# Performance work log

Hardware: AMD Instinct MI355X
Metric: run time of the kernel (lower is better)

Reference implementation:

```python
import jax, jax.numpy as jnp
import numpy as np
from jax import lax

B, C, H, W, P = 16, 256, 64, 64, 4
EPS = 1e-5


def setup_inputs() -> dict:
    key = jax.random.key(0)
    ks = jax.random.split(key, 16)
    s = 0.05
    d = {
        'rgb': jax.random.normal(ks[0], (B, C, H, W), jnp.float32),
        'th': jax.random.normal(ks[1], (B, C, H, W), jnp.float32),
        'q_w': jax.random.normal(ks[2], (C, C), jnp.float32) * s,
        'q_b': jax.random.normal(ks[3], (C,), jnp.float32) * s,
        'kvr_w': jax.random.normal(ks[4], (2 * C, C), jnp.float32) * s,
        'kvr_b': jax.random.normal(ks[5], (2 * C,), jnp.float32) * s,
        'kvt_w': jax.random.normal(ks[6], (2 * C, C), jnp.float32) * s,
        'kvt_b': jax.random.normal(ks[7], (2 * C,), jnp.float32) * s,
        'offr_w': jax.random.normal(ks[8], (2 * P, C, 3, 3), jnp.float32) * s,
        'offr_b': jax.random.normal(ks[9], (2 * P,), jnp.float32) * s,
        'offt_w': jax.random.normal(ks[10], (2 * P, C, 3, 3), jnp.float32) * s,
        'offt_b': jax.random.normal(ks[11], (2 * P,), jnp.float32) * s,
        'out_w': jax.random.normal(ks[12], (C, 2 * C), jnp.float32) * s,
        'out_b': jax.random.normal(ks[13], (C,), jnp.float32) * s,
        'gamma': jnp.ones((C,), jnp.float32),
        'beta': jnp.zeros((C,), jnp.float32),
    }
    return d


def conv1x1(x, w, b):
    # x: [B,Ci,H,W], w: [Co,Ci] -> [B,Co,H,W]
    return jnp.einsum('bchw,oc->bohw', x, w) + b[None, :, None, None]


def conv3x3(x, w, b):
    y = lax.conv_general_dilated(x, w, (1, 1), 'SAME',
                                 dimension_numbers=('NCHW', 'OIHW', 'NCHW'))
    return y + b[None, :, None, None]


def deform_sample(feat, offset):
    # feat: [B,C,H,W]; offset: [B,2P,H,W] (pixel-unit offsets, (x,y) pairs)
    Bs, Cs, Hs, Ws = feat.shape
    off = offset.reshape(Bs, -1, 2, Hs, Ws)  # [B,P,2,H,W]
    # base grid in [-1,1], align_corners=True convention
    gy = jnp.linspace(-1.0, 1.0, Hs)[None, None, :, None]
    gx = jnp.linspace(-1.0, 1.0, Ws)[None, None, None, :]
    grid_x = gx + off[:, :, 0] / (Ws / 2.0)  # [B,P,H,W]
    grid_y = gy + off[:, :, 1] / (Hs / 2.0)
    # normalized -> pixel coords (align_corners=True)
    x = (grid_x + 1.0) * (Ws - 1) / 2.0
    y = (grid_y + 1.0) * (Hs - 1) / 2.0
    x0 = jnp.floor(x)
    y0 = jnp.floor(y)
    wx = x - x0
    wy = y - y0
    feat_flat = feat.reshape(Bs, Cs, Hs * Ws)

    def corner(xi, yi, wgt):
        valid = (xi >= 0) & (xi < Ws) & (yi >= 0) & (yi < Hs)  # zeros padding
        xc = jnp.clip(xi, 0, Ws - 1).astype(jnp.int32)
        yc = jnp.clip(yi, 0, Hs - 1).astype(jnp.int32)
        idx = (yc * Ws + xc).reshape(Bs, 1, -1)  # [B,1,P*H*W]
        g = jnp.take_along_axis(feat_flat, jnp.broadcast_to(idx, (Bs, Cs, idx.shape[-1])), axis=2)
        g = g.reshape(Bs, Cs, -1, Hs, Ws)  # [B,C,P,H,W]
        w_eff = (wgt * valid.astype(feat.dtype))[:, None]  # [B,1,P,H,W]
        return g * w_eff

    x0i = x0.astype(jnp.int32)
    y0i = y0.astype(jnp.int32)
    out = (corner(x0i, y0i, (1 - wx) * (1 - wy))
           + corner(x0i + 1, y0i, wx * (1 - wy))
           + corner(x0i, y0i + 1, (1 - wx) * wy)
           + corner(x0i + 1, y0i + 1, wx * wy))
    return out.mean(axis=2)  # mean over P -> [B,C,H,W]


def batchnorm_train(x, gamma, beta):
    mu = x.mean(axis=(0, 2, 3), keepdims=True)
    var = x.var(axis=(0, 2, 3), keepdims=True)
    xn = (x - mu) * lax.rsqrt(var + EPS)
    return xn * gamma[None, :, None, None] + beta[None, :, None, None]


def reference(rgb, th, q_w, q_b, kvr_w, kvr_b, kvt_w, kvt_b,
              offr_w, offr_b, offt_w, offt_b, out_w, out_b, gamma, beta):
    q_rgb = conv1x1(rgb, q_w, q_b)
    q_th = conv1x1(th, q_w, q_b)
    kv_rgb = conv1x1(rgb, kvr_w, kvr_b)
    kv_th = conv1x1(th, kvt_w, kvt_b)
    v_rgb = kv_rgb[:, C:]  # k_rgb = kv_rgb[:, :C] is unused downstream
    v_th = kv_th[:, C:]
    off_rgb2th = conv3x3(th, offr_w, offr_b)
    off_th2rgb = conv3x3(rgb, offt_w, offt_b)
    v_rgb2th = deform_sample(v_rgb, off_rgb2th)
    v_th2rgb = deform_sample(v_th, off_th2rgb)
    attn_rgb = jax.nn.sigmoid(q_rgb) * v_th2rgb
    attn_th = jax.nn.sigmoid(q_th) * v_rgb2th
    fused = conv1x1(jnp.concatenate([attn_rgb, attn_th], axis=1), out_w, out_b)
    return batchnorm_train(fused + 0.5 * (rgb + th), gamma, beta)
```

## Files before the change

### kernel.cpp

```cpp
#include <hip/hip_runtime.h>

typedef __bf16 bf16x8 __attribute__((ext_vector_type(8)));
typedef float  f32x4  __attribute__((ext_vector_type(4)));

constexpr int Bn = 16, Cn = 256, Hn = 64, Wn = 64, HWn = 64 * 64;
constexpr int Ntot = Bn * HWn;

#define DEV static __device__ __forceinline__

DEV unsigned short f2bf(float f) {
  unsigned u = __builtin_bit_cast(unsigned, f);
  u += 0x7fffu + ((u >> 16) & 1u);
  return (unsigned short)(u >> 16);
}
DEV float bf2f(unsigned short s) {
  unsigned u = ((unsigned)s) << 16;
  return __builtin_bit_cast(float, u);
}
DEV bf16x8 asbf(uint4 u) { return __builtin_bit_cast(bf16x8, u); }

__global__ void k_prep(const float* qw, const float* kvrw, const float* kvtw,
                       const float* offrw, const float* offtw, const float* outw,
                       unsigned short* Aqv, unsigned short* Aoff, unsigned short* Aout) {
  int idx = blockIdx.x * 256 + threadIdx.x;
  if (idx < 2 * 512 * 256) {
    int t = idx >> 17; int r = idx & 131071; int o = r >> 8; int c = r & 255;
    float v = (o < 256) ? qw[o * 256 + c] : (t ? kvtw[o * 256 + c] : kvrw[o * 256 + c]);
    Aqv[idx] = f2bf(v);
    return;
  }
  idx -= 2 * 512 * 256;
  if (idx < 2 * 16 * 2304) {
    int t = idx / 36864; int r = idx % 36864;
    int o = r / 2304; int rc = r % 2304; int tap = rc >> 8; int c = rc & 255;
    const float* w = t ? offtw : offrw;
    float v = (o < 8) ? w[(o * 256 + c) * 9 + tap] : 0.f;
    Aoff[idx] = f2bf(v);
    return;
  }
  idx -= 2 * 16 * 2304;
  if (idx < 256 * 512) Aout[idx] = f2bf(outw[idx]);
}

__global__ void k_transpose(const float* rgb, const float* th, unsigned short* xT) {
  int bi = blockIdx.x;
  int ct = bi & 3;
  int nt = (bi >> 2) & 63;
  int b  = (bi >> 8) & 15;
  int t  = bi >> 12;
  const float* src = t ? th : rgb;
  int c0 = ct * 64, n0 = nt * 64;
  __shared__ float tile[64][65];
  int tid = threadIdx.x;
  int nl = tid & 63, cg = tid >> 6;
#pragma unroll
  for (int i = 0; i < 16; i++) {
    int c = cg * 16 + i;
    tile[c][nl] = src[(size_t)(b * 256 + c0 + c) * HWn + n0 + nl];
  }
  __syncthreads();
  int pr = tid >> 2, sg = tid & 3;
  unsigned short tmp[16];
#pragma unroll
  for (int j = 0; j < 16; j++) tmp[j] = f2bf(tile[sg * 16 + j][pr]);
  unsigned short* dst = xT + (size_t)t * Ntot * 256 +
                        (size_t)(b * HWn + n0 + pr) * 256 + c0 + sg * 16;
  *(uint4*)(dst)     = *(const uint4*)(tmp);
  *(uint4*)(dst + 8) = *(const uint4*)(tmp + 8);
}

__global__ __launch_bounds__(512, 2) void k_qv(
    const unsigned short* Aqv, const unsigned short* xT,
    const float* qb, const float* kvrb, const float* kvtb,
    unsigned short* qs, unsigned short* vv) {
  __shared__ unsigned short smem[32768];
  int t  = blockIdx.z;
  int mt = blockIdx.y;
  int nt = blockIdx.x;
  int swznt = ((nt & 7) << 6) | (nt >> 3);
  int o0 = mt * 128;
  int n0 = swznt * 128;
  int tid = threadIdx.x;
  const unsigned short* Aq = Aqv + t * 512 * 256;
  const unsigned short* Xg = xT + (size_t)t * Ntot * 256 + (size_t)n0 * 256;

  auto stage = [&](int kb, int bb) {
    unsigned short* As = smem + bb * 8192;
    unsigned short* Xs = smem + 16384 + bb * 8192;
#pragma unroll
    for (int i = 0; i < 2; i++) {
      int cid = tid + i * 512;
      int row = cid >> 3, seg = cid & 7;
      int ss = seg ^ (row & 7);
      *(uint4*)(&As[row * 64 + seg * 8]) =
          *(const uint4*)(Aq + (size_t)(o0 + row) * 256 + kb * 64 + ss * 8);
    }
#pragma unroll
    for (int i = 0; i < 2; i++) {
      int cid = tid + i * 512;
      int row = cid >> 3, seg = cid & 7;
      int ss = seg ^ (row & 7);
      *(uint4*)(&Xs[row * 64 + seg * 8]) =
          *(const uint4*)(Xg + (size_t)row * 256 + kb * 64 + ss * 8);
    }
  };

  int w = __builtin_amdgcn_readfirstlane(tid >> 6);
  int lane = tid & 63;
  int wo = w & 1, wn = w >> 1;
  int r16 = lane & 15, q4 = lane >> 4;

  f32x4 acc[4][2];
#pragma unroll
  for (int a = 0; a < 4; a++) { acc[a][0] = f32x4{0.f,0.f,0.f,0.f}; acc[a][1] = f32x4{0.f,0.f,0.f,0.f}; }

  stage(0, 0);
  __syncthreads();
#pragma unroll
  for (int kb = 0; kb < 4; kb++) {
    if (kb < 3) stage(kb + 1, (kb + 1) & 1);
    const unsigned short* As = smem + (kb & 1) * 8192;
    const unsigned short* Xs = smem + 16384 + (kb & 1) * 8192;
#pragma unroll
    for (int ks = 0; ks < 2; ks++) {
      uint4 af[4], bfr[2];
#pragma unroll
      for (int oi = 0; oi < 4; oi++) {
        int row = wo * 64 + oi * 16 + r16;
        int seg = (ks * 4 + q4) ^ (row & 7);
        af[oi] = *(const uint4*)(&As[row * 64 + seg * 8]);
      }
#pragma unroll
      for (int ni = 0; ni < 2; ni++) {
        int row = wn * 32 + ni * 16 + r16;
        int seg = (ks * 4 + q4) ^ (row & 7);
        bfr[ni] = *(const uint4*)(&Xs[row * 64 + seg * 8]);
      }
#pragma unroll
      for (int oi = 0; oi < 4; oi++)
#pragma unroll
        for (int ni = 0; ni < 2; ni++)
          acc[oi][ni] = __builtin_amdgcn_mfma_f32_16x16x32_bf16(
              asbf(af[oi]), asbf(bfr[ni]), acc[oi][ni], 0, 0, 0);
    }
    __syncthreads();
  }

  bool isq = (mt < 2);
  const float* bias = isq ? qb : (t ? kvtb : kvrb);
  float4 bv[4];
#pragma unroll
  for (int oi = 0; oi < 4; oi++)
    bv[oi] = *(const float4*)(&bias[o0 + wo * 64 + oi * 16 + q4 * 4]);
#pragma unroll
  for (int oi = 0; oi < 4; oi++) {
    int ol = wo * 64 + oi * 16 + q4 * 4;
#pragma unroll
    for (int ni = 0; ni < 2; ni++) {
      int nl = wn * 32 + ni * 16 + r16;
      unsigned short pk[4];
#pragma unroll
      for (int j = 0; j < 4; j++) {
        float val = acc[oi][ni][j] + ((const float*)&bv[oi])[j];
        if (isq) val = 1.f / (1.f + __expf(-val));
        pk[j] = f2bf(val);
      }
      *(uint2*)(&smem[nl * 132 + ol]) = *(const uint2*)(pk);
    }
  }
  __syncthreads();
  unsigned short* outp = (isq ? qs : vv) + (size_t)t * Ntot * 256 + (mt & 1) * 128;
#pragma unroll
  for (int pass = 0; pass < 4; pass++) {
    int nl = pass * 32 + (tid >> 4);
    int c  = tid & 15;
    uint4 vq = *(const uint4*)(&smem[nl * 132 + c * 8]);
    *(uint4*)(outp + (size_t)(n0 + nl) * 256 + c * 8) = vq;
  }
}

__global__ void k_off(const unsigned short* Aoff, const unsigned short* xT,
                      const float* offrb, const float* offtb, float* offo) {
  int t  = blockIdx.y;
  int bh = blockIdx.x;
  int b = bh >> 6, h = bh & 63;
  int tid = threadIdx.x, lane = tid & 63, w = tid >> 6;
  int r16 = lane & 15, q4 = lane >> 4;
  int wl = w * 16 + r16;
  const unsigned short* Aw  = Aoff + t * 36864;
  const unsigned short* xin = xT + (size_t)(t ? 0 : 1) * Ntot * 256;
  f32x4 acc = {0.f, 0.f, 0.f, 0.f};
#pragma unroll
  for (int tap = 0; tap < 9; tap++) {
    int dy = tap / 3 - 1, dx = tap % 3 - 1;
    int hh = h + dy, ww = wl + dx;
    bool valid = (hh >= 0 && hh < 64 && ww >= 0 && ww < 64);
    const unsigned short* bsrc =
        xin + (size_t)((b * 64 + (valid ? hh : 0)) * 64 + (valid ? ww : 0)) * 256 + q4 * 8;
#pragma unroll
    for (int ks = 0; ks < 8; ks++) {
      uint4 a = *(const uint4*)(Aw + (r16 * 9 + tap) * 256 + ks * 32 + q4 * 8);
      uint4 bv;
      if (valid) bv = *(const uint4*)(bsrc + ks * 32);
      else { bv.x = 0; bv.y = 0; bv.z = 0; bv.w = 0; }
      acc = __builtin_amdgcn_mfma_f32_16x16x32_bf16(asbf(a), asbf(bv), acc, 0, 0, 0);
    }
  }
  if (lane < 32) {
    const float* ob = t ? offtb : offrb;
    int n = (b * 64 + h) * 64 + wl;
    float4 r;
    r.x = acc[0] + ob[q4 * 4 + 0];
    r.y = acc[1] + ob[q4 * 4 + 1];
    r.z = acc[2] + ob[q4 * 4 + 2];
    r.w = acc[3] + ob[q4 * 4 + 3];
    *(float4*)(offo + (size_t)t * Ntot * 8 + (size_t)n * 8 + q4 * 4) = r;
  }
}

__global__ void k_gather(const unsigned short* qs, const unsigned short* vv,
                         const float* offo, unsigned short* concat) {
  int tid = threadIdx.x;
  int bi  = blockIdx.x;
  int pass = blockIdx.y;
  int swz = ((bi & 7) << 9) | (bi >> 3);
  int chunk = tid & 15, pixL = tid >> 4;
  int n = swz * 16 + pixL;
  int b = n >> 12;
  int h = (n >> 6) & 63, pix = n & 63;
  const unsigned short* vsrc = vv + (size_t)(pass ? 0 : 1) * Ntot * 256;
  const float* offp          = offo + (size_t)(pass ? 0 : 1) * Ntot * 8;
  const unsigned short* qsrc = qs + (size_t)(pass ? 1 : 0) * Ntot * 256;
  float acc[16];
#pragma unroll
  for (int i = 0; i < 16; i++) acc[i] = 0.f;
#pragma unroll
  for (int p = 0; p < 4; p++) {
    float dx = offp[(size_t)n * 8 + 2 * p], dy = offp[(size_t)n * 8 + 2 * p + 1];
    float xf = (float)pix + dx * (63.f / 64.f);
    float yf = (float)h   + dy * (63.f / 64.f);
    float x0f = floorf(xf), y0f = floorf(yf);
    float wx = xf - x0f, wy = yf - y0f;
    int x0 = (int)x0f, y0 = (int)y0f;
#pragma unroll
    for (int cc = 0; cc < 4; cc++) {
      int cy = cc >> 1, cx = cc & 1;
      int ix = x0 + cx, iy = y0 + cy;
      bool ok = (ix >= 0 && ix < 64 && iy >= 0 && iy < 64);
      int ixc = ix < 0 ? 0 : (ix > 63 ? 63 : ix);
      int iyc = iy < 0 ? 0 : (iy > 63 ? 63 : iy);
      float wgt = (cx ? wx : 1.f - wx) * (cy ? wy : 1.f - wy);
      wgt = ok ? wgt : 0.f;
      const unsigned short* g =
          vsrc + (size_t)(((b * 64 + iyc) * 64 + ixc) * 256 + chunk * 16);
      uint4 raw0 = *(const uint4*)(g);
      uint4 raw1 = *(const uint4*)(g + 8);
      const unsigned short* r0 = (const unsigned short*)&raw0;
      const unsigned short* r1 = (const unsigned short*)&raw1;
#pragma unroll
      for (int e = 0; e < 8; e++) {
        acc[e]     += wgt * bf2f(r0[e]);
        acc[8 + e] += wgt * bf2f(r1[e]);
      }
    }
  }
  uint4 q0 = *(const uint4*)(qsrc + (size_t)n * 256 + chunk * 16);
  uint4 q1 = *(const uint4*)(qsrc + (size_t)n * 256 + chunk * 16 + 8);
  const unsigned short* qp0 = (const unsigned short*)&q0;
  const unsigned short* qp1 = (const unsigned short*)&q1;
  unsigned short pk[16];
#pragma unroll
  for (int e = 0; e < 8; e++) {
    pk[e]     = f2bf(0.25f * acc[e]     * bf2f(qp0[e]));
    pk[8 + e] = f2bf(0.25f * acc[8 + e] * bf2f(qp1[e]));
  }
  unsigned short* dst = concat + (size_t)n * 512 + pass * 256 + chunk * 16;
  *(uint4*)(dst)     = *(const uint4*)(pk);
  *(uint4*)(dst + 8) = *(const uint4*)(pk + 8);
}

__global__ __launch_bounds__(512, 2) void k_out(
    const unsigned short* Aout, const unsigned short* concat, const float* outb,
    const float* rgb, const float* th, float* dout, float* partial) {
  __shared__ unsigned short Asm[2][128 * 64];
  __shared__ unsigned short Xsm[2][128 * 64];
  __shared__ float bstat[128][2];
  int bi = blockIdx.x;
  int my = blockIdx.y;
  int swz = ((bi & 7) << 6) | (bi >> 3);
  int n0 = swz * 128;
  int o0 = my * 128;
  int tid = threadIdx.x;
  if (tid < 128) { bstat[tid][0] = 0.f; bstat[tid][1] = 0.f; }

  auto stage = [&](int kb, int bb) {
#pragma unroll
    for (int i = 0; i < 2; i++) {
      int cid = tid + i * 512;
      int row = cid >> 3, seg = cid & 7;
      int ss = seg ^ (row & 7);
      *(uint4*)(&Asm[bb][row * 64 + seg * 8]) =
          *(const uint4*)(Aout + (size_t)(o0 + row) * 512 + kb * 64 + ss * 8);
    }
#pragma unroll
    for (int i = 0; i < 2; i++) {
      int cid = tid + i * 512;
      int row = cid >> 3, seg = cid & 7;
      int ss = seg ^ (row & 7);
      *(uint4*)(&Xsm[bb][row * 64 + seg * 8]) =
          *(const uint4*)(concat + (size_t)(n0 + row) * 512 + kb * 64 + ss * 8);
    }
  };

  int w = __builtin_amdgcn_readfirstlane(tid >> 6);
  int lane = tid & 63;
  int wo = w & 1, wn = w >> 1;
  int r16 = lane & 15, q4 = lane >> 4;

  f32x4 acc2[4][2];
#pragma unroll
  for (int a = 0; a < 4; a++) { acc2[a][0] = f32x4{0.f,0.f,0.f,0.f}; acc2[a][1] = f32x4{0.f,0.f,0.f,0.f}; }

  stage(0, 0);
  __syncthreads();
#pragma unroll
  for (int kb = 0; kb < 8; kb++) {
    if (kb < 7) stage(kb + 1, (kb + 1) & 1);
    int bb = kb & 1;
#pragma unroll
    for (int ks = 0; ks < 2; ks++) {
      uint4 af[4], bfr[2];
#pragma unroll
      for (int oi = 0; oi < 4; oi++) {
        int row = wo * 64 + oi * 16 + r16;
        int seg = (ks * 4 + q4) ^ (row & 7);
        af[oi] = *(const uint4*)(&Asm[bb][row * 64 + seg * 8]);
      }
#pragma unroll
      for (int ni = 0; ni < 2; ni++) {
        int row = wn * 32 + ni * 16 + r16;
        int seg = (ks * 4 + q4) ^ (row & 7);
        bfr[ni] = *(const uint4*)(&Xsm[bb][row * 64 + seg * 8]);
      }
#pragma unroll
      for (int oi = 0; oi < 4; oi++)
#pragma unroll
        for (int ni = 0; ni < 2; ni++)
          acc2[oi][ni] = __builtin_amdgcn_mfma_f32_16x16x32_bf16(
              asbf(af[oi]), asbf(bfr[ni]), acc2[oi][ni], 0, 0, 0);
    }
    __syncthreads();
  }
#pragma unroll
  for (int oi = 0; oi < 4; oi++) {
    int obl = wo * 64 + oi * 16 + q4 * 4;
#pragma unroll
    for (int j = 0; j < 4; j++) {
      int ol = obl + j;
      int o = o0 + ol;
      float s1 = 0.f, s2 = 0.f;
#pragma unroll
      for (int ni = 0; ni < 2; ni++) {
        int pl = wn * 32 + ni * 16 + r16;
        int n = n0 + pl;
        int bI = n >> 12, hw = n & 4095;
        size_t gidx = (size_t)(bI * 256 + o) * HWn + hw;
        float val = acc2[oi][ni][j] + outb[o] + 0.5f * (rgb[gidx] + th[gidx]);
        dout[gidx] = val;
        s1 += val; s2 += val * val;
      }
#pragma unroll
      for (int m = 1; m < 16; m <<= 1) {
        s1 += __shfl_xor(s1, m, 16);
        s2 += __shfl_xor(s2, m, 16);
      }
      if (r16 == 0) { atomicAdd(&bstat[ol][0], s1); atomicAdd(&bstat[ol][1], s2); }
    }
  }
  __syncthreads();
  if (tid < 128) {
    partial[((size_t)my * 512 + bi) * 256 + tid]       = bstat[tid][0];
    partial[((size_t)my * 512 + bi) * 256 + 128 + tid] = bstat[tid][1];
  }
}

__global__ void k_stats(const float* partial, const float* gamma, const float* beta,
                        float* sstats) {
  int c = blockIdx.x, tid = threadIdx.x;
  int my = c >> 7, j = c & 127;
  float s1 = 0.f, s2 = 0.f;
  for (int i = tid; i < 512; i += 256) {
    const float* pp = partial + ((size_t)my * 512 + i) * 256;
    s1 += pp[j];
    s2 += pp[128 + j];
  }
  __shared__ float r1[256], r2[256];
  r1[tid] = s1; r2[tid] = s2;
  __syncthreads();
  for (int st = 128; st > 0; st >>= 1) {
    if (tid < st) { r1[tid] += r1[tid + st]; r2[tid] += r2[tid + st]; }
    __syncthreads();
  }
  if (tid == 0) {
    float mean = r1[0] / 65536.f;
    float var  = r2[0] / 65536.f - mean * mean;
    float scale = gamma[c] / sqrtf(var + 1e-5f);
    sstats[c]       = scale;
    sstats[256 + c] = beta[c] - mean * scale;
  }
}

__global__ void k_bn(float* dout, const float* sstats) {
  int idx = blockIdx.x * 256 + threadIdx.x;
  size_t base = (size_t)idx * 4;
  int c = (int)((base >> 12) & 255);
  float4 v = *(float4*)(dout + base);
  float sc = sstats[c], sh = sstats[256 + c];
  v.x = v.x * sc + sh; v.y = v.y * sc + sh;
  v.z = v.z * sc + sh; v.w = v.w * sc + sh;
  *(float4*)(dout + base) = v;
}

extern "C" void kernel_launch(void* const* d_in, const int* in_sizes, int n_in,
                              void* d_out, int out_size, void* d_ws, size_t ws_size,
                              hipStream_t stream) {
  const float* rgb   = (const float*)d_in[0];
  const float* th    = (const float*)d_in[1];
  const float* qw    = (const float*)d_in[2];
  const float* qb    = (const float*)d_in[3];
  const float* kvrw  = (const float*)d_in[4];
  const float* kvrb  = (const float*)d_in[5];
  const float* kvtw  = (const float*)d_in[6];
  const float* kvtb  = (const float*)d_in[7];
  const float* offrw = (const float*)d_in[8];
  const float* offrb = (const float*)d_in[9];
  const float* offtw = (const float*)d_in[10];
  const float* offtb = (const float*)d_in[11];
  const float* outw  = (const float*)d_in[12];
  const float* outb  = (const float*)d_in[13];
  const float* gamma = (const float*)d_in[14];
  const float* beta  = (const float*)d_in[15];
  float* dout = (float*)d_out;

  unsigned short* xT   = (unsigned short*)d_ws;
  unsigned short* qsb  = xT  + (size_t)2 * Ntot * 256;
  unsigned short* vvb  = qsb + (size_t)2 * Ntot * 256;
  float* offo          = (float*)(vvb + (size_t)2 * Ntot * 256);
  unsigned short* Aqv  = (unsigned short*)(offo + (size_t)2 * Ntot * 8);
  unsigned short* Aoff = Aqv + 2 * 512 * 256;
  unsigned short* Aout = Aoff + 2 * 16 * 2304;
  float* partial       = (float*)(Aout + 256 * 512);
  float* sstats        = partial + (size_t)1024 * 256;
  unsigned short* concat = xT;

  k_prep<<<1824, 256, 0, stream>>>(qw, kvrw, kvtw, offrw, offtw, outw, Aqv, Aoff, Aout);
  k_transpose<<<8192, 256, 0, stream>>>(rgb, th, xT);
  k_qv<<<dim3(512, 4, 2), 512, 0, stream>>>(Aqv, xT, qb, kvrb, kvtb, qsb, vvb);
  k_off<<<dim3(1024, 2), 256, 0, stream>>>(Aoff, xT, offrb, offtb, offo);
  k_gather<<<dim3(4096, 2), 256, 0, stream>>>(qsb, vvb, offo, concat);
  k_out<<<dim3(512, 2), 512, 0, stream>>>(Aout, concat, outb, rgb, th, dout, partial);
  k_stats<<<256, 256, 0, stream>>>(partial, gamma, beta, sstats);
  k_bn<<<16384, 256, 0, stream>>>(dout, sstats);
}
```

Before: 460.8 us.

## Stage offset-conv weights in LDS and double-buffer input tap loads

The 3x3 offset convolution kernel now copies its 8-output-channel weight slice into shared memory once per block. Rows 9-15 of the MFMA A operand read from a zero pad in LDS, so those lanes no longer issue global weight loads. Input tap loads are software-pipelined across two register buffers, so the next tap's global reads overlap the current tap's MFMAs. Block indices are swizzled and launch bounds are set. The trade-off is higher register pressure from the two buffers and about 38KB of LDS per block, which may limit occupancy.

```diff
diff --git a/kernel.cpp b/kernel.cpp
--- a/kernel.cpp
+++ b/kernel.cpp
@@ -179,33 +179,86 @@
   }
 }
 
-__global__ void k_off(const unsigned short* Aoff, const unsigned short* xT,
-                      const float* offrb, const float* offtb, float* offo) {
+__global__ __launch_bounds__(256, 4) void k_off(
+    const unsigned short* Aoff, const unsigned short* xT,
+    const float* offrb, const float* offtb, float* offo) {
+  __shared__ unsigned short Alds[9 * 8 * 264 + 264];
   int t  = blockIdx.y;
   int bh = blockIdx.x;
-  int b = bh >> 6, h = bh & 63;
-  int tid = threadIdx.x, lane = tid & 63, w = tid >> 6;
+  int swz = ((bh & 7) << 7) | (bh >> 3);
+  int b = swz >> 6, h = swz & 63;
+  int tid = threadIdx.x;
+  const unsigned short* Aw = Aoff + t * 36864;
+
+#pragma unroll
+  for (int i = 0; i < 9; i++) {
+    int cid = tid + i * 256;
+    int o = cid / 288;
+    int rem = cid - o * 288;
+    int tap = rem >> 5, cg = rem & 31;
+    uint4 v = *(const uint4*)(Aw + o * 2304 + tap * 256 + cg * 8);
+    *(uint4*)(&Alds[(tap * 8 + o) * 264 + cg * 8]) = v;
+  }
+  if (tid < 33) {
+    uint4 z; z.x = 0; z.y = 0; z.z = 0; z.w = 0;
+    *(uint4*)(&Alds[19008 + tid * 8]) = z;
+  }
+  __syncthreads();
+
+  int lane = tid & 63, w = tid >> 6;
   int r16 = lane & 15, q4 = lane >> 4;
   int wl = w * 16 + r16;
-  const unsigned short* Aw  = Aoff + t * 36864;
   const unsigned short* xin = xT + (size_t)(t ? 0 : 1) * Ntot * 256;
+  int zbase = 19008 + q4 * 8;
+  int abase = r16 * 264 + q4 * 8;
+  bool rowok = (r16 < 8);
+
   f32x4 acc = {0.f, 0.f, 0.f, 0.f};
-#pragma unroll
-  for (int tap = 0; tap < 9; tap++) {
-    int dy = tap / 3 - 1, dx = tap % 3 - 1;
-    int hh = h + dy, ww = wl + dx;
-    bool valid = (hh >= 0 && hh < 64 && ww >= 0 && ww < 64);
-    const unsigned short* bsrc =
-        xin + (size_t)((b * 64 + (valid ? hh : 0)) * 64 + (valid ? ww : 0)) * 256 + q4 * 8;
-#pragma unroll
-    for (int ks = 0; ks < 8; ks++) {
-      uint4 a = *(const uint4*)(Aw + (r16 * 9 + tap) * 256 + ks * 32 + q4 * 8);
-      uint4 bv;
-      if (valid) bv = *(const uint4*)(bsrc + ks * 32);
-      else { bv.x = 0; bv.y = 0; bv.z = 0; bv.w = 0; }
-      acc = __builtin_amdgcn_mfma_f32_16x16x32_bf16(asbf(a), asbf(bv), acc, 0, 0, 0);
-    }
-  }
+  uint4 bufA[8], bufB[8];
+
+#define LOADT(buf, tap) {                                                      \
+    int dy = (tap) / 3 - 1, dx = (tap) % 3 - 1;                                \
+    int hh = h + dy, ww = wl + dx;                                             \
+    bool ok = (hh >= 0 && hh < 64 && ww >= 0 && ww < 64);                      \
+    int hc = hh < 0 ? 0 : (hh > 63 ? 63 : hh);                                 \
+    int wc = ww < 0 ? 0 : (ww > 63 ? 63 : ww);                                 \
+    const unsigned short* p =                                                  \
+        xin + (size_t)(((b * 64 + hc) * 64 + wc) * 256) + q4 * 8;              \
+    _Pragma("unroll") for (int ks = 0; ks < 8; ks++) {                         \
+      uint4 v = *(const uint4*)(p + ks * 32);                                  \
+      if (!ok) { v.x = 0; v.y = 0; v.z = 0; v.w = 0; }                         \
+      buf[ks] = v;                                                             \
+    } }
+
+#define COMPT(buf, tap) {                                                      \
+    _Pragma("unroll") for (int ks = 0; ks < 8; ks++) {                         \
+      int aofs = rowok ? ((tap) * 8 * 264 + abase + ks * 32) : (zbase + ks * 32); \
+      uint4 af = *(const uint4*)(&Alds[aofs]);                                 \
+      acc = __builtin_amdgcn_mfma_f32_16x16x32_bf16(asbf(af), asbf(buf[ks]),   \
+                                                    acc, 0, 0, 0);             \
+    } }
+
+  LOADT(bufA, 0)
+  LOADT(bufB, 1)
+  COMPT(bufA, 0)
+  LOADT(bufA, 2)
+  COMPT(bufB, 1)
+  LOADT(bufB, 3)
+  COMPT(bufA, 2)
+  LOADT(bufA, 4)
+  COMPT(bufB, 3)
+  LOADT(bufB, 5)
+  COMPT(bufA, 4)
+  LOADT(bufA, 6)
+  COMPT(bufB, 5)
+  LOADT(bufB, 7)
+  COMPT(bufA, 6)
+  LOADT(bufA, 8)
+  COMPT(bufB, 7)
+  COMPT(bufA, 8)
+#undef LOADT
+#undef COMPT
+
   if (lane < 32) {
     const float* ob = t ? offtb : offrb;
     int n = (b * 64 + h) * 64 + wl;
```

New measurement: 406.2 us. -11.8%, faster.
